# Kernel optimization log

Hardware: AMD Instinct MI355X
Metric: run time of the kernel (lower is better)

Reference implementation:

```python
import jax, jax.numpy as jnp
import numpy as np

B = 4; D = H = W = 28; C = 192; NH = 6; WS = 7; SS = 3
L = D * H * W; N = WS ** 3; HD = C // NH


def _rel_index():
    c = np.stack(np.meshgrid(np.arange(WS), np.arange(WS), np.arange(WS), indexing='ij')).reshape(3, -1)
    r = c[:, :, None] - c[:, None, :] + (WS - 1)
    return jnp.asarray(r[0] * (2 * WS - 1) ** 2 + r[1] * (2 * WS - 1) + r[2])  # (N,N)


def _attn_mask():
    img = np.zeros((D, H, W), np.float32)
    sl = (slice(0, -WS), slice(-WS, -SS), slice(-SS, None))
    cnt = 0
    for d in sl:
        for h in sl:
            for w in sl:
                img[d, h, w] = cnt; cnt += 1
    mw = img.reshape(D // WS, WS, H // WS, WS, W // WS, WS).transpose(0, 2, 4, 1, 3, 5).reshape(-1, N)
    am = mw[:, None, :] - mw[:, :, None]
    return jnp.asarray(np.where(am != 0, -100.0, 0.0).astype(np.float32))  # (nW,N,N)

REL_IDX = _rel_index()
ATTN_MASK = _attn_mask()


def _ln(x, g, b):
    m = x.mean(-1, keepdims=True)
    v = ((x - m) ** 2).mean(-1, keepdims=True)
    return (x - m) / jnp.sqrt(v + 1e-5) * g + b


def _window_partition(x):  # (B,D,H,W,C) -> (B*nW, N, C)
    x = x.reshape(B, D // WS, WS, H // WS, WS, W // WS, WS, C)
    return x.transpose(0, 1, 3, 5, 2, 4, 6, 7).reshape(-1, N, C)


def _window_reverse(w):  # (B*nW, N, C) -> (B,D,H,W,C)
    x = w.reshape(B, D // WS, H // WS, W // WS, WS, WS, WS, C)
    return x.transpose(0, 1, 4, 2, 5, 3, 6, 7).reshape(B, D, H, W, C)


def setup_inputs() -> dict:
    key = jax.random.key(0)
    ks = jax.random.split(key, 8)
    s = 0.02
    return {
        'x': jax.random.normal(ks[0], (B, L, C), jnp.float32),
        'norm1_g': jnp.ones((C,), jnp.float32), 'norm1_b': jnp.zeros((C,), jnp.float32),
        'qkv_w': jax.random.normal(ks[1], (3 * C, C), jnp.float32) * s,
        'qkv_b': jnp.zeros((3 * C,), jnp.float32),
        'proj_w': jax.random.normal(ks[2], (C, C), jnp.float32) * s,
        'proj_b': jnp.zeros((C,), jnp.float32),
        'rel_table': jax.random.normal(ks[3], ((2 * WS - 1) ** 3, NH), jnp.float32) * s,
        'norm2_g': jnp.ones((C,), jnp.float32), 'norm2_b': jnp.zeros((C,), jnp.float32),
        'fc1_w': jax.random.normal(ks[4], (4 * C, C), jnp.float32) * s,
        'fc1_b': jnp.zeros((4 * C,), jnp.float32),
        'fc2_w': jax.random.normal(ks[5], (C, 4 * C), jnp.float32) * s,
        'fc2_b': jnp.zeros((C,), jnp.float32),
    }


def reference(x, norm1_g, norm1_b, qkv_w, qkv_b, proj_w, proj_b, rel_table,
              norm2_g, norm2_b, fc1_w, fc1_b, fc2_w, fc2_b):
    shortcut = x
    h = _ln(x, norm1_g, norm1_b).reshape(B, D, H, W, C)
    h = jnp.roll(h, (-SS, -SS, -SS), axis=(1, 2, 3))
    xw = _window_partition(h)                                  # (B_, N, C)
    B_ = xw.shape[0]
    qkv = (xw @ qkv_w.T + qkv_b).reshape(B_, N, 3, NH, HD).transpose(2, 0, 3, 1, 4)
    q, k, v = qkv[0], qkv[1], qkv[2]                           # (B_, NH, N, HD)
    attn = jnp.einsum('bhnd,bhmd->bhnm', q * (HD ** -0.5), k)
    bias = rel_table[REL_IDX].transpose(2, 0, 1)               # (NH, N, N)
    attn = attn + bias[None]
    nW = ATTN_MASK.shape[0]
    attn = (attn.reshape(B, nW, NH, N, N) + ATTN_MASK[None, :, None]).reshape(B_, NH, N, N)
    attn = jax.nn.softmax(attn, axis=-1)
    out = jnp.einsum('bhnm,bhmd->bhnd', attn, v).transpose(0, 2, 1, 3).reshape(B_, N, C)
    out = out @ proj_w.T + proj_b
    h = _window_reverse(out)
    h = jnp.roll(h, (SS, SS, SS), axis=(1, 2, 3)).reshape(B, L, C)
    x = shortcut + h
    y = _ln(x, norm2_g, norm2_b)
    y = jax.nn.gelu(y @ fc1_w.T + fc1_b, approximate=False)
    return x + (y @ fc2_w.T + fc2_b)
```

## Files before the change

### kernel.cpp

```cpp
#include <hip/hip_runtime.h>

#define DEV __device__ __forceinline__

typedef __bf16 bf16x8 __attribute__((ext_vector_type(8)));
typedef float f32x4 __attribute__((ext_vector_type(4)));

DEV float bflo(unsigned int u) { union { unsigned int x; float f; } c; c.x = u << 16; return c.f; }
DEV unsigned short f2bf(float f) {
  union { float f; unsigned int u; } c; c.f = f;
  unsigned int u = c.u;
  return (unsigned short)((u + 0x7fffu + ((u >> 16) & 1u)) >> 16);
}
DEV unsigned int pkbf(float a, float b) {
  unsigned int r;
  asm("v_cvt_pk_bf16_f32 %0, %1, %2" : "=v"(r) : "v"(a), "v"(b));
  return r;
}
DEV float gelu_fast(float y) {
  float y2 = y * y;
  float z = y * fmaf(y2, 0.10294348f, 2.30220842f);
  float e = __builtin_amdgcn_exp2f(z);
  float r = __builtin_amdgcn_rcpf(e + 1.0f);
  return fmaf(-y, r, y);
}

DEV void gload16(const void* g, void* l) {
  __builtin_amdgcn_global_load_lds((const __attribute__((address_space(1))) void*)g,
                                   (__attribute__((address_space(3))) void*)l, 16, 0, 0);
}

__global__ __launch_bounds__(256) void wconv_all(const float* __restrict__ s0,
                                                 const float* __restrict__ s1,
                                                 const float* __restrict__ s2,
                                                 const float* __restrict__ s3,
                                                 unsigned short* __restrict__ dst) {
  int i = blockIdx.x * 256 + threadIdx.x;
  const float* src; int off, real;
  if (i < 122880)      { src = s0; off = i;          real = 110592; }
  else if (i < 172032) { src = s1; off = i - 122880; real = 36864; }
  else if (i < 319488) { src = s2; off = i - 172032; real = 147456; }
  else                 { src = s3; off = i - 319488; real = 147456; }
  dst[i] = (off < real) ? f2bf(src[off]) : (unsigned short)0;
}

__global__ __launch_bounds__(256) void bmt_kernel(const float* __restrict__ rel_table,
                                                  unsigned short* __restrict__ bmt4) {
  int wth = blockIdx.x;
  int wt = wth / 6, h = wth - wt * 6;
  int r = blockIdx.y;
  unsigned short* row = bmt4 + (((size_t)wth * 88 + r) * 352) * 4;
  for (int q = threadIdx.x; q < 352; q += 256) {
    int mb_q = 0, cls_q = 0;
    bool qv = q < 343;
    if (qv) {
      int ii_q = q / 49, rem_q = q - ii_q * 49;
      int jj_q = rem_q / 7, ww_q = rem_q - jj_q * 7;
      mb_q = ii_q * 169 + jj_q * 13 + ww_q;
      int cd_q = (wt & 4) ? (ii_q < 4 ? 1 : 2) : 0;
      int ch_q = (wt & 2) ? (jj_q < 4 ? 1 : 2) : 0;
      int cw_q = (wt & 1) ? (ww_q < 4 ? 1 : 2) : 0;
      cls_q = cd_q * 9 + ch_q * 3 + cw_q;
    }
    unsigned short ov[4];
#pragma unroll
    for (int i = 0; i < 4; i++) {
      int kk = 4 * r + i;
      float v;
      if (kk >= 343) v = -30000.f;
      else if (!qv) v = 0.f;
      else {
        int ii_k = kk / 49, rem_k = kk - ii_k * 49;
        int jj_k = rem_k / 7, ww_k = rem_k - jj_k * 7;
        int mb_k = ii_k * 169 + jj_k * 13 + ww_k;
        int cd_k = (wt & 4) ? (ii_k < 4 ? 1 : 2) : 0;
        int ch_k = (wt & 2) ? (jj_k < 4 ? 1 : 2) : 0;
        int cw_k = (wt & 1) ? (ww_k < 4 ? 1 : 2) : 0;
        int cls_k = cd_k * 9 + ch_k * 3 + cw_k;
        v = rel_table[(mb_q - mb_k + 1098) * 6 + h] * 1.4426950408889634f;
        if (cls_q != cls_k) v -= 144.26950408889634f;
      }
      ov[i] = f2bf(v);
    }
    unsigned int lo = (unsigned)ov[0] | ((unsigned)ov[1] << 16);
    unsigned int hi = (unsigned)ov[2] | ((unsigned)ov[3] << 16);
    *(uint2*)(row + q * 4) = make_uint2(lo, hi);
  }
}

__global__ __launch_bounds__(256) void ln_kernel(const float* __restrict__ x,
                                                 const float* __restrict__ g,
                                                 const float* __restrict__ b,
                                                 unsigned short* __restrict__ out) {
  int row = (blockIdx.x << 2) + (threadIdx.x >> 6);
  int lane = threadIdx.x & 63;
  int w_ = row / 343, n_ = row - w_ * 343;
  int bb = w_ >> 6, wrem = w_ & 63;
  int wd = wrem >> 4, wh = (wrem >> 2) & 3, ww = wrem & 3;
  int ii = n_ / 49, rem = n_ - ii * 49;
  int jj = rem / 7, kk = rem - jj * 7;
  int d = wd * 7 + ii + 3; if (d >= 28) d -= 28;
  int hh = wh * 7 + jj + 3; if (hh >= 28) hh -= 28;
  int wb = ww * 7 + kk + 3; if (wb >= 28) wb -= 28;
  const float* xr = x + ((size_t)bb * 21952 + (d * 28 + hh) * 28 + wb) * 192;
  float v0 = xr[lane], v1 = xr[lane + 64], v2 = xr[lane + 128];
  float s = v0 + v1 + v2;
  float sq = v0 * v0 + v1 * v1 + v2 * v2;
#pragma unroll
  for (int o = 32; o > 0; o >>= 1) {
    s += __shfl_xor(s, o, 64);
    sq += __shfl_xor(sq, o, 64);
  }
  float mean = s * (1.0f / 192.0f);
  float var = sq * (1.0f / 192.0f) - mean * mean;
  float rstd = rsqrtf(var + 1e-5f);
  unsigned short* orow = out + (size_t)row * 192;
  orow[lane]       = f2bf((v0 - mean) * rstd * g[lane] + b[lane]);
  orow[lane + 64]  = f2bf((v1 - mean) * rstd * g[lane + 64] + b[lane + 64]);
  orow[lane + 128] = f2bf((v2 - mean) * rstd * g[lane + 128] + b[lane + 128]);
}

__global__ __launch_bounds__(256) void gemm_qkv(
    const unsigned short* __restrict__ A, const unsigned short* __restrict__ W,
    const float* __restrict__ bias,
    unsigned short* __restrict__ oq, unsigned short* __restrict__ okk,
    unsigned short* __restrict__ ov) {
  __shared__ __align__(16) unsigned short As[2][128 * 64];
  __shared__ __align__(16) unsigned short Bs[2][128 * 64];
  const int K = 192;
  const int orig = blockIdx.x;
  const int xcd = orig & 7, off = orig >> 3;
  const int wgid = (xcd < 6 ? xcd * 429 : 2574 + (xcd - 6) * 428) + off;
  const int by = wgid / 5, bx = wgid - by * 5;
  const int bm = by << 7, bn = bx << 7;

  const int tid = threadIdx.x;
  const int lane = tid & 63;
  const int wv = tid >> 6;
  const int wr = wv >> 1, wc = wv & 1;
  const int l15 = lane & 15, l4 = lane >> 4;
  const int srow = lane >> 3;
  const int scole = ((lane & 7) ^ srow) << 3;

  f32x4 acc[4][4];
#pragma unroll
  for (int a = 0; a < 4; a++)
#pragma unroll
    for (int b2 = 0; b2 < 4; b2++) acc[a][b2] = (f32x4){0.f, 0.f, 0.f, 0.f};

  auto stage = [&](int kt, int buf) {
#pragma unroll
    for (int i = 0; i < 4; i++) {
      int c = (i << 2) + wv;
      int row = (c << 3) + srow;
      gload16(A + (size_t)(bm + row) * K + (kt << 6) + scole, &As[buf][c << 9]);
      gload16(W + (size_t)(bn + row) * K + (kt << 6) + scole, &Bs[buf][c << 9]);
    }
  };

  stage(0, 0);
  int cur = 0;
  for (int kt = 0; kt < 3; ++kt) {
    if (kt < 2) {
      stage(kt + 1, cur ^ 1);
      asm volatile("s_waitcnt vmcnt(8)" ::: "memory");
    } else {
      asm volatile("s_waitcnt vmcnt(0)" ::: "memory");
    }
    __builtin_amdgcn_s_barrier();
    __builtin_amdgcn_sched_barrier(0);
#pragma unroll
    for (int ks = 0; ks < 2; ks++) {
      bf16x8 af[4], bfr[4];
#pragma unroll
      for (int fm = 0; fm < 4; fm++) {
        int r = (wr << 6) + (fm << 4) + l15;
        int c = (ks << 2) + l4;
        af[fm] = *(const bf16x8*)(&As[cur][(r << 6) + ((c ^ (r & 7)) << 3)]);
      }
#pragma unroll
      for (int fn = 0; fn < 4; fn++) {
        int r = (wc << 6) + (fn << 4) + l15;
        int c = (ks << 2) + l4;
        bfr[fn] = *(const bf16x8*)(&Bs[cur][(r << 6) + ((c ^ (r & 7)) << 3)]);
      }
#pragma unroll
      for (int fm = 0; fm < 4; fm++)
#pragma unroll
        for (int fn = 0; fn < 4; fn++)
          acc[fm][fn] = __builtin_amdgcn_mfma_f32_16x16x32_bf16(bfr[fn], af[fm], acc[fm][fn], 0, 0, 0);
    }
    if (kt < 2) {
      __builtin_amdgcn_sched_barrier(0);
      __builtin_amdgcn_s_barrier();
      cur ^= 1;
    }
  }

#pragma unroll
  for (int fm = 0; fm < 4; fm++) {
    int gr = bm + (wr << 6) + (fm << 4) + l15;
    int w_ = gr / 343, n_ = gr - w_ * 343;
#pragma unroll
    for (int fn = 0; fn < 4; fn++) {
      int gc0 = bn + (wc << 6) + (fn << 4) + (l4 << 2);
      if (gc0 < 576) {
        float4 bv = *(const float4*)(bias + gc0);
        float v0 = acc[fm][fn][0] + bv.x, v1 = acc[fm][fn][1] + bv.y;
        float v2 = acc[fm][fn][2] + bv.z, v3 = acc[fm][fn][3] + bv.w;
        int which = gc0 / 192;
        int cc3 = gc0 - which * 192;
        int hh2 = cc3 >> 5, dd0 = cc3 & 31;
        size_t offo = ((size_t)(w_ * 6 + hh2) * 343 + n_) * 32 + dd0;
        if (which == 0) {
          const float sc = 0.17677669529663687f * 1.4426950408889634f;
          *(uint2*)(oq + offo) = make_uint2(pkbf(v0 * sc, v1 * sc), pkbf(v2 * sc, v3 * sc));
        } else if (which == 1) {
          *(uint2*)(okk + offo) = make_uint2(pkbf(v0, v1), pkbf(v2, v3));
        } else {
          *(uint2*)(ov + offo) = make_uint2(pkbf(v0, v1), pkbf(v2, v3));
        }
      }
    }
  }
}

__global__ __launch_bounds__(256) void proj_mlp(
    const unsigned short* __restrict__ A,
    const unsigned short* __restrict__ Wp, const float* __restrict__ bp,
    const float* __restrict__ x,
    const float* __restrict__ g2, const float* __restrict__ b2,
    const unsigned short* __restrict__ W1, const float* __restrict__ b1,
    const unsigned short* __restrict__ W2, const float* __restrict__ b2b,
    float* __restrict__ out) {
  __shared__ __align__(16) char smem[43008];
  unsigned short* pBs  = (unsigned short*)smem;
  unsigned short* pAs  = (unsigned short*)(smem + 24576);
  unsigned short* xw2s = (unsigned short*)smem;
  unsigned short* Hs   = (unsigned short*)(smem + 24576);
  float* red = (float*)(smem + 24576);

  const int tid = threadIdx.x, lane = tid & 63, wv = tid >> 6;
  const int l15 = lane & 15, l4 = lane >> 4;
  const int bm = blockIdx.x << 6;

  f32x4 acc[4][3];
#pragma unroll
  for (int a = 0; a < 4; a++)
#pragma unroll
    for (int b_ = 0; b_ < 3; b_++) acc[a][b_] = (f32x4){0.f, 0.f, 0.f, 0.f};

  for (int kt = 0; kt < 3; ++kt) {
    __syncthreads();
#pragma unroll
    for (int i = 0; i < 2; i++) {
      int u = (i << 8) + tid;
      int r = u >> 3, ch = u & 7;
      gload16(A + (size_t)(bm + r) * 192 + (kt << 6) + ((ch ^ (r & 7)) << 3), pAs + (u << 3));
    }
#pragma unroll
    for (int i = 0; i < 6; i++) {
      int u = (i << 8) + tid;
      int r = u >> 3, ch = u & 7;
      gload16(Wp + (size_t)r * 192 + (kt << 6) + ((ch ^ (r & 7)) << 3), pBs + (u << 3));
    }
    asm volatile("s_waitcnt vmcnt(0)" ::: "memory");
    __syncthreads();
#pragma unroll
    for (int ks = 0; ks < 2; ks++) {
      bf16x8 af[4], bfr[3];
#pragma unroll
      for (int fm = 0; fm < 4; fm++) {
        int r = (fm << 4) + l15;
        int c = (ks << 2) + l4;
        af[fm] = *(const bf16x8*)(pAs + (r << 6) + ((c ^ (r & 7)) << 3));
      }
#pragma unroll
      for (int fn = 0; fn < 3; fn++) {
        int rr = wv * 48 + (fn << 4) + l15;
        int c = (ks << 2) + l4;
        bfr[fn] = *(const bf16x8*)(pBs + (rr << 6) + ((c ^ (rr & 7)) << 3));
      }
#pragma unroll
      for (int fm = 0; fm < 4; fm++)
#pragma unroll
        for (int fn = 0; fn < 3; fn++)
          acc[fm][fn] = __builtin_amdgcn_mfma_f32_16x16x32_bf16(bfr[fn], af[fm], acc[fm][fn], 0, 0, 0);
    }
  }

  int orow[4];
#pragma unroll
  for (int fm = 0; fm < 4; fm++) {
    int gr = bm + (fm << 4) + l15;
    int w_ = gr / 343, n_ = gr - w_ * 343;
    int bb = w_ >> 6, wrem = w_ & 63;
    int wd = wrem >> 4, wh = (wrem >> 2) & 3, ww = wrem & 3;
    int ii = n_ / 49, rem = n_ - ii * 49;
    int jj = rem / 7, kk = rem - jj * 7;
    int d = wd * 7 + ii + 3; if (d >= 28) d -= 28;
    int hh = wh * 7 + jj + 3; if (hh >= 28) hh -= 28;
    int wb = ww * 7 + kk + 3; if (wb >= 28) wb -= 28;
    orow[fm] = ((bb * 21952 + (d * 28 + hh) * 28 + wb) * 192);
  }
  float ps[4], psq[4];
#pragma unroll
  for (int fm = 0; fm < 4; fm++) {
    float s = 0.f, sq = 0.f;
#pragma unroll
    for (int fn = 0; fn < 3; fn++) {
      int gc0 = wv * 48 + (fn << 4) + (l4 << 2);
      float4 bv = *(const float4*)(bp + gc0);
      float4 xv = *(const float4*)(x + (size_t)orow[fm] + gc0);
      acc[fm][fn][0] += bv.x + xv.x;
      acc[fm][fn][1] += bv.y + xv.y;
      acc[fm][fn][2] += bv.z + xv.z;
      acc[fm][fn][3] += bv.w + xv.w;
#pragma unroll
      for (int i = 0; i < 4; i++) {
        float v = acc[fm][fn][i];
        s += v; sq += v * v;
      }
    }
    ps[fm] = s; psq[fm] = sq;
  }
#pragma unroll
  for (int fm = 0; fm < 4; fm++) {
    ps[fm] += __shfl_xor(ps[fm], 16, 64);
    ps[fm] += __shfl_xor(ps[fm], 32, 64);
    psq[fm] += __shfl_xor(psq[fm], 16, 64);
    psq[fm] += __shfl_xor(psq[fm], 32, 64);
  }
  __syncthreads();
  if (l4 == 0) {
#pragma unroll
    for (int fm = 0; fm < 4; fm++) {
      int tr = (fm << 4) + l15;
      red[tr * 8 + wv] = ps[fm];
      red[tr * 8 + 4 + wv] = psq[fm];
    }
  }
  __syncthreads();
  if (tid < 64) {
    float s = red[tid * 8] + red[tid * 8 + 1] + red[tid * 8 + 2] + red[tid * 8 + 3];
    float sq = red[tid * 8 + 4] + red[tid * 8 + 5] + red[tid * 8 + 6] + red[tid * 8 + 7];
    float mean = s * (1.0f / 192.0f);
    float var = sq * (1.0f / 192.0f) - mean * mean;
    red[tid * 8] = mean;
    red[tid * 8 + 1] = rsqrtf(var + 1e-5f);
  }
  __syncthreads();
  unsigned int xnb[4][3][2];
#pragma unroll
  for (int fm = 0; fm < 4; fm++) {
    int tr = (fm << 4) + l15;
    float mean = red[tr * 8], rstd = red[tr * 8 + 1];
#pragma unroll
    for (int fn = 0; fn < 3; fn++) {
      int gc0 = wv * 48 + (fn << 4) + (l4 << 2);
      float4 gv = *(const float4*)(g2 + gc0);
      float4 b2v = *(const float4*)(b2 + gc0);
      float v0 = acc[fm][fn][0], v1 = acc[fm][fn][1];
      float v2 = acc[fm][fn][2], v3 = acc[fm][fn][3];
      xnb[fm][fn][0] = pkbf(v0, v1);
      xnb[fm][fn][1] = pkbf(v2, v3);
      float y0 = (v0 - mean) * rstd * gv.x + b2v.x;
      float y1 = (v1 - mean) * rstd * gv.y + b2v.y;
      float y2 = (v2 - mean) * rstd * gv.z + b2v.z;
      float y3 = (v3 - mean) * rstd * gv.w + b2v.w;
      int ch = gc0 >> 3;
      *(uint2*)(xw2s + tr * 192 + ((ch ^ (tr & 7)) << 3) + (gc0 & 7)) =
          make_uint2(pkbf(y0, y1), pkbf(y2, y3));
    }
  }
  __syncthreads();

  f32x4 acc2[4][3];
#pragma unroll
  for (int a = 0; a < 4; a++)
#pragma unroll
    for (int b_ = 0; b_ < 3; b_++) acc2[a][b_] = (f32x4){0.f, 0.f, 0.f, 0.f};

  for (int cc = 0; cc < 6; cc++) {
    f32x4 acc1[4][2];
#pragma unroll
    for (int a = 0; a < 4; a++) {
      acc1[a][0] = (f32x4){0.f, 0.f, 0.f, 0.f};
      acc1[a][1] = (f32x4){0.f, 0.f, 0.f, 0.f};
    }
#pragma unroll
    for (int ks = 0; ks < 6; ks++) {
      bf16x8 af[4], w1f[2];
#pragma unroll
      for (int fm = 0; fm < 4; fm++) {
        int r = (fm << 4) + l15;
        int ch = (ks << 2) + l4;
        af[fm] = *(const bf16x8*)(xw2s + r * 192 + ((ch ^ (r & 7)) << 3));
      }
#pragma unroll
      for (int fn = 0; fn < 2; fn++) {
        int hrow = (cc << 7) + (wv << 5) + (fn << 4) + l15;
        w1f[fn] = *(const bf16x8*)(W1 + (size_t)hrow * 192 + (ks << 5) + (l4 << 3));
      }
#pragma unroll
      for (int fm = 0; fm < 4; fm++)
#pragma unroll
        for (int fn = 0; fn < 2; fn++)
          acc1[fm][fn] = __builtin_amdgcn_mfma_f32_16x16x32_bf16(w1f[fn], af[fm], acc1[fm][fn], 0, 0, 0);
    }
    __syncthreads();
#pragma unroll
    for (int fm = 0; fm < 4; fm++) {
      int r = (fm << 4) + l15;
#pragma unroll
      for (int fn = 0; fn < 2; fn++) {
        int hc = (wv << 5) + (fn << 4) + (l4 << 2);
        float4 bv = *(const float4*)(b1 + (cc << 7) + hc);
        float g0 = gelu_fast(acc1[fm][fn][0] + bv.x);
        float g1 = gelu_fast(acc1[fm][fn][1] + bv.y);
        float g2_ = gelu_fast(acc1[fm][fn][2] + bv.z);
        float g3 = gelu_fast(acc1[fm][fn][3] + bv.w);
        *(uint2*)(Hs + r * 136 + hc) = make_uint2(pkbf(g0, g1), pkbf(g2_, g3));
      }
    }
    __syncthreads();
#pragma unroll
    for (int ks = 0; ks < 4; ks++) {
      bf16x8 hf[4], w2f[3];
#pragma unroll
      for (int fm = 0; fm < 4; fm++) {
        int r = (fm << 4) + l15;
        hf[fm] = *(const bf16x8*)(Hs + r * 136 + (ks << 5) + (l4 << 3));
      }
#pragma unroll
      for (int fn = 0; fn < 3; fn++) {
        int j = wv * 48 + (fn << 4) + l15;
        w2f[fn] = *(const bf16x8*)(W2 + (size_t)j * 768 + (cc << 7) + (ks << 5) + (l4 << 3));
      }
#pragma unroll
      for (int fm = 0; fm < 4; fm++)
#pragma unroll
        for (int fn = 0; fn < 3; fn++)
          acc2[fm][fn] = __builtin_amdgcn_mfma_f32_16x16x32_bf16(w2f[fn], hf[fm], acc2[fm][fn], 0, 0, 0);
    }
  }

#pragma unroll
  for (int fm = 0; fm < 4; fm++) {
#pragma unroll
    for (int fn = 0; fn < 3; fn++) {
      int gc0 = wv * 48 + (fn << 4) + (l4 << 2);
      float4 bv = *(const float4*)(b2b + gc0);
      float4 o;
      o.x = acc2[fm][fn][0] + bv.x + bflo(xnb[fm][fn][0] & 0xffffu);
      o.y = acc2[fm][fn][1] + bv.y + bflo(xnb[fm][fn][0] >> 16);
      o.z = acc2[fm][fn][2] + bv.z + bflo(xnb[fm][fn][1] & 0xffffu);
      o.w = acc2[fm][fn][3] + bv.w + bflo(xnb[fm][fn][1] >> 16);
      *(float4*)(out + (size_t)orow[fm] + gc0) = o;
    }
  }
}

__global__ __launch_bounds__(256) void attn_mfma(const unsigned short* __restrict__ q,
                                                 const unsigned short* __restrict__ k,
                                                 const unsigned short* __restrict__ v,
                                                 const unsigned short* __restrict__ bmt4,
                                                 unsigned short* __restrict__ out) {
  __shared__ __align__(16) unsigned short Ks[352 * 32];
  __shared__ __align__(16) unsigned short Vt[32 * 360];

  const int blk = blockIdx.x;
  const int h_ = blk >> 8;
  const int idx = blk & 255;
  const int cums[8] = {0, 108, 144, 180, 192, 228, 240, 252};
  int c = (idx >= 108) + (idx >= 144) + (idx >= 180) + (idx >= 192) +
          (idx >= 228) + (idx >= 240) + (idx >= 252);
  int r0 = idx - cums[c];
  int sh = (c & 2) ? 1 : 3, sw = (c & 1) ? 1 : 3;
  int p = ((c & 4) ? 1 : 3) * sh * sw;
  int b = r0 / p, q2 = r0 - b * p;
  int wd, wh, ww;
  if (c & 4) wd = 3; else { wd = q2 / (sh * sw); q2 -= wd * sh * sw; }
  if (c & 2) wh = 3; else { wh = q2 / sw; q2 -= wh * sw; }
  ww = (c & 1) ? 3 : q2;
  const int w_ = b * 64 + wd * 16 + wh * 4 + ww;
  const int wt = c;
  const int blkqkv = w_ * 6 + h_;

  const int t = threadIdx.x, lane = t & 63, wv = t >> 6;
  const int l15 = lane & 15, l4 = lane >> 4;
  const unsigned short* Qb = q + (size_t)blkqkv * (343 * 32);
  const unsigned short* Kb = k + (size_t)blkqkv * (343 * 32);
  const unsigned short* Vb = v + (size_t)blkqkv * (343 * 32);
  const unsigned short* bm4 = bmt4 + ((size_t)(wt * 6 + h_) * 88) * 352 * 4;

  for (int cc = t; cc < 1408; cc += 256) {
    int r = cc >> 2, ch = cc & 3;
    int swc = ch ^ ((r >> 1) & 3);
    uint4 val = make_uint4(0, 0, 0, 0);
    if (r < 343) val = *(const uint4*)(Kb + r * 32 + ch * 8);
    *(uint4*)(Ks + r * 32 + swc * 8) = val;
  }
#pragma unroll
  for (int ch = 0; ch < 4; ch++) {
    for (int n = t; n < 343; n += 256) {
      union { uint4 u4; unsigned short us[8]; } val;
      val.u4 = *(const uint4*)(Vb + n * 32 + ch * 8);
#pragma unroll
      for (int j = 0; j < 8; j++) Vt[(ch * 8 + j) * 360 + n] = val.us[j];
    }
  }
  for (int cc = t; cc < 288; cc += 256) {
    int d = cc / 9, n = 343 + (cc - d * 9);
    Vt[d * 360 + n] = 0;
  }
  __syncthreads();

  const int ksw = (l4 ^ ((l15 >> 1) & 3)) << 3;

  for (int tq = wv; tq < 22; tq += 4) {
    int qrow = tq * 16 + l15; if (qrow > 342) qrow = 342;
    bf16x8 qf = *(const bf16x8*)(Qb + qrow * 32 + l4 * 8);

    unsigned int u0[22], u1[22];
    float lsum = 0.f;
#pragma unroll
    for (int kt = 0; kt < 22; kt++) {
      bf16x8 kf = *(const bf16x8*)(Ks + (kt * 16 + l15) * 32 + ksw);
      f32x4 s = __builtin_amdgcn_mfma_f32_16x16x32_bf16(kf, qf, (f32x4){0.f, 0.f, 0.f, 0.f}, 0, 0, 0);
      const unsigned short* bp = bm4 + ((size_t)((kt << 2) + l4) * 352 + (tq << 4) + l15) * 4;
      uint2 bv = *(const uint2*)bp;
      float p0 = __builtin_amdgcn_exp2f(s[0] + bflo(bv.x & 0xffffu));
      float p1 = __builtin_amdgcn_exp2f(s[1] + bflo(bv.x >> 16));
      float p2 = __builtin_amdgcn_exp2f(s[2] + bflo(bv.y & 0xffffu));
      float p3 = __builtin_amdgcn_exp2f(s[3] + bflo(bv.y >> 16));
      lsum += (p0 + p1) + (p2 + p3);
      asm("v_cvt_pk_bf16_f32 %0, %1, %2" : "=v"(u0[kt]) : "v"(p0), "v"(p1));
      asm("v_cvt_pk_bf16_f32 %0, %1, %2" : "=v"(u1[kt]) : "v"(p2), "v"(p3));
    }
    lsum += __shfl_xor(lsum, 16, 64);
    lsum += __shfl_xor(lsum, 32, 64);
    float inv = 1.0f / lsum;

    f32x4 oacc0 = (f32x4){0.f, 0.f, 0.f, 0.f};
    f32x4 oacc1 = (f32x4){0.f, 0.f, 0.f, 0.f};
#pragma unroll
    for (int ck = 0; ck < 11; ck++) {
      unsigned int dw[4];
#pragma unroll
      for (int d = 0; d < 4; d++) {
        int src = l15 + 16 * ((d >> 1) + 2 * (l4 & 1));
        unsigned int x = __shfl((d & 1) ? u1[2 * ck] : u0[2 * ck], src, 64);
        unsigned int y = __shfl((d & 1) ? u1[2 * ck + 1] : u0[2 * ck + 1], src, 64);
        dw[d] = (l4 < 2) ? x : y;
      }
      union { unsigned int u[4]; bf16x8 v; } pc;
      pc.u[0] = dw[0]; pc.u[1] = dw[1]; pc.u[2] = dw[2]; pc.u[3] = dw[3];
      bf16x8 vf0 = *(const bf16x8*)(Vt + (size_t)l15 * 360 + ck * 32 + l4 * 8);
      bf16x8 vf1 = *(const bf16x8*)(Vt + (size_t)(16 + l15) * 360 + ck * 32 + l4 * 8);
      oacc0 = __builtin_amdgcn_mfma_f32_16x16x32_bf16(vf0, pc.v, oacc0, 0, 0, 0);
      oacc1 = __builtin_amdgcn_mfma_f32_16x16x32_bf16(vf1, pc.v, oacc1, 0, 0, 0);
    }

    int qg = tq * 16 + l15;
    if (qg < 343) {
      unsigned short* orow = out + ((size_t)w_ * 343 + qg) * 192 + h_ * 32;
      *(uint2*)(orow + (l4 << 2)) =
          make_uint2(pkbf(oacc0[0] * inv, oacc0[1] * inv), pkbf(oacc0[2] * inv, oacc0[3] * inv));
      *(uint2*)(orow + 16 + (l4 << 2)) =
          make_uint2(pkbf(oacc1[0] * inv, oacc1[1] * inv), pkbf(oacc1[2] * inv, oacc1[3] * inv));
    }
  }
}

extern "C" void kernel_launch(void* const* d_in, const int* in_sizes, int n_in,
                              void* d_out, int out_size, void* d_ws, size_t ws_size,
                              hipStream_t stream) {
  const float* x      = (const float*)d_in[0];
  const float* n1g    = (const float*)d_in[1];
  const float* n1b    = (const float*)d_in[2];
  const float* qkv_w  = (const float*)d_in[3];
  const float* qkv_b  = (const float*)d_in[4];
  const float* proj_w = (const float*)d_in[5];
  const float* proj_b = (const float*)d_in[6];
  const float* rel_t  = (const float*)d_in[7];
  const float* n2g    = (const float*)d_in[8];
  const float* n2b    = (const float*)d_in[9];
  const float* fc1_w  = (const float*)d_in[10];
  const float* fc1_b  = (const float*)d_in[11];
  const float* fc2_w  = (const float*)d_in[12];
  const float* fc2_b  = (const float*)d_in[13];

  char* ws = (char*)d_ws;
  if (ws_size < 147820032ull) return;
  unsigned short* WQKV  = (unsigned short*)(ws);
  unsigned short* WPROJ = (unsigned short*)(ws + 245760);
  unsigned short* WFC1  = (unsigned short*)(ws + 344064);
  unsigned short* WFC2  = (unsigned short*)(ws + 638976);
  unsigned short* XW    = (unsigned short*)(ws + 1032192);
  unsigned short* Q_    = (unsigned short*)(ws + 34750464);
  unsigned short* K_    = (unsigned short*)(ws + 68468736);
  unsigned short* V_    = (unsigned short*)(ws + 102187008);
  unsigned short* BMT4  = (unsigned short*)(ws + 135925248);
  float* OUT = (float*)d_out;

  wconv_all<<<2016, 256, 0, stream>>>(qkv_w, proj_w, fc1_w, fc2_w, WQKV);

  bmt_kernel<<<dim3(48, 88), 256, 0, stream>>>(rel_t, BMT4);

  ln_kernel<<<21952, 256, 0, stream>>>(x, n1g, n1b, XW);

  gemm_qkv<<<3430, 256, 0, stream>>>(XW, WQKV, qkv_b, Q_, K_, V_);

  attn_mfma<<<1536, 256, 0, stream>>>(Q_, K_, V_, BMT4, XW);

  proj_mlp<<<1372, 256, 0, stream>>>(XW, WPROJ, proj_b, x, n2g, n2b,
                                     WFC1, fc1_b, WFC2, fc2_b, OUT);
}
```

Before: 326.1 us.

## Double-buffer MLP hidden tile and prefetch W1/W2 fragments into registers

The MLP hidden-chunk buffer in shared memory is split into two alternating buffers, which removes one barrier per chunk. W1 and W2 fragments for each chunk are loaded into registers up front, so global loads can overlap the MFMA and GELU work. The chunk loop is fully unrolled and the kernel asks for two blocks per SIMD through launch bounds. In exchange it uses more LDS and many more VGPRs, which risks spills or lower occupancy.

```diff
diff --git a/kernel.cpp b/kernel.cpp
--- a/kernel.cpp
+++ b/kernel.cpp
@@ -224,7 +224,7 @@
   }
 }
 
-__global__ __launch_bounds__(256) void proj_mlp(
+__global__ __launch_bounds__(256, 2) void proj_mlp(
     const unsigned short* __restrict__ A,
     const unsigned short* __restrict__ Wp, const float* __restrict__ bp,
     const float* __restrict__ x,
@@ -232,11 +232,12 @@
     const unsigned short* __restrict__ W1, const float* __restrict__ b1,
     const unsigned short* __restrict__ W2, const float* __restrict__ b2b,
     float* __restrict__ out) {
-  __shared__ __align__(16) char smem[43008];
+  __shared__ __align__(16) char smem[59392];
   unsigned short* pBs  = (unsigned short*)smem;
   unsigned short* pAs  = (unsigned short*)(smem + 24576);
   unsigned short* xw2s = (unsigned short*)smem;
-  unsigned short* Hs   = (unsigned short*)(smem + 24576);
+  unsigned short* Hs0  = (unsigned short*)(smem + 24576);
+  unsigned short* Hs1  = (unsigned short*)(smem + 41984);
   float* red = (float*)(smem + 24576);
 
   const int tid = threadIdx.x, lane = tid & 63, wv = tid >> 6;
@@ -380,7 +381,17 @@
 #pragma unroll
     for (int b_ = 0; b_ < 3; b_++) acc2[a][b_] = (f32x4){0.f, 0.f, 0.f, 0.f};
 
+#pragma unroll
   for (int cc = 0; cc < 6; cc++) {
+    unsigned short* Hc = (cc & 1) ? Hs1 : Hs0;
+    bf16x8 w1r[2][6];
+#pragma unroll
+    for (int fn = 0; fn < 2; fn++)
+#pragma unroll
+      for (int ks = 0; ks < 6; ks++) {
+        int hrow = (cc << 7) + (wv << 5) + (fn << 4) + l15;
+        w1r[fn][ks] = *(const bf16x8*)(W1 + (size_t)hrow * 192 + (ks << 5) + (l4 << 3));
+      }
     f32x4 acc1[4][2];
 #pragma unroll
     for (int a = 0; a < 4; a++) {
@@ -389,7 +400,7 @@
     }
 #pragma unroll
     for (int ks = 0; ks < 6; ks++) {
-      bf16x8 af[4], w1f[2];
+      bf16x8 af[4];
 #pragma unroll
       for (int fm = 0; fm < 4; fm++) {
         int r = (fm << 4) + l15;
@@ -397,17 +408,19 @@
         af[fm] = *(const bf16x8*)(xw2s + r * 192 + ((ch ^ (r & 7)) << 3));
       }
 #pragma unroll
-      for (int fn = 0; fn < 2; fn++) {
-        int hrow = (cc << 7) + (wv << 5) + (fn << 4) + l15;
-        w1f[fn] = *(const bf16x8*)(W1 + (size_t)hrow * 192 + (ks << 5) + (l4 << 3));
-      }
-#pragma unroll
       for (int fm = 0; fm < 4; fm++)
 #pragma unroll
         for (int fn = 0; fn < 2; fn++)
-          acc1[fm][fn] = __builtin_amdgcn_mfma_f32_16x16x32_bf16(w1f[fn], af[fm], acc1[fm][fn], 0, 0, 0);
-    }
-    __syncthreads();
+          acc1[fm][fn] = __builtin_amdgcn_mfma_f32_16x16x32_bf16(w1r[fn][ks], af[fm], acc1[fm][fn], 0, 0, 0);
+    }
+    bf16x8 w2r[3][4];
+#pragma unroll
+    for (int fn = 0; fn < 3; fn++)
+#pragma unroll
+      for (int ks = 0; ks < 4; ks++) {
+        int j = wv * 48 + (fn << 4) + l15;
+        w2r[fn][ks] = *(const bf16x8*)(W2 + (size_t)j * 768 + (cc << 7) + (ks << 5) + (l4 << 3));
+      }
 #pragma unroll
     for (int fm = 0; fm < 4; fm++) {
       int r = (fm << 4) + l15;
@@ -419,28 +432,23 @@
         float g1 = gelu_fast(acc1[fm][fn][1] + bv.y);
         float g2_ = gelu_fast(acc1[fm][fn][2] + bv.z);
         float g3 = gelu_fast(acc1[fm][fn][3] + bv.w);
-        *(uint2*)(Hs + r * 136 + hc) = make_uint2(pkbf(g0, g1), pkbf(g2_, g3));
+        *(uint2*)(Hc + r * 136 + hc) = make_uint2(pkbf(g0, g1), pkbf(g2_, g3));
       }
     }
     __syncthreads();
 #pragma unroll
     for (int ks = 0; ks < 4; ks++) {
-      bf16x8 hf[4], w2f[3];
+      bf16x8 hf[4];
 #pragma unroll
       for (int fm = 0; fm < 4; fm++) {
         int r = (fm << 4) + l15;
-        hf[fm] = *(const bf16x8*)(Hs + r * 136 + (ks << 5) + (l4 << 3));
-      }
-#pragma unroll
-      for (int fn = 0; fn < 3; fn++) {
-        int j = wv * 48 + (fn << 4) + l15;
-        w2f[fn] = *(const bf16x8*)(W2 + (size_t)j * 768 + (cc << 7) + (ks << 5) + (l4 << 3));
+        hf[fm] = *(const bf16x8*)(Hc + r * 136 + (ks << 5) + (l4 << 3));
       }
 #pragma unroll
       for (int fm = 0; fm < 4; fm++)
 #pragma unroll
         for (int fn = 0; fn < 3; fn++)
-          acc2[fm][fn] = __builtin_amdgcn_mfma_f32_16x16x32_bf16(w2f[fn], hf[fm], acc2[fm][fn], 0, 0, 0);
+          acc2[fm][fn] = __builtin_amdgcn_mfma_f32_16x16x32_bf16(w2r[fn][ks], hf[fm], acc2[fm][fn], 0, 0, 0);
     }
   }
 
```

Measured after the change: 314.5 us. -3.6%, faster.

## Stage full proj A tile in LDS once and read proj weights from global

Applied to the files above, without the earlier changes.

The projection GEMM in proj_mlp no longer loops over three K-tiles that each stage A and Wp slices in shared memory. It now loads the whole 64x192 A tile into LDS once, swizzled to match the later xw2 layout, and reads Wp fragments straight from global/L2. The residual x loads are issued early so they overlap the MFMA loop. Shared memory shrinks slightly and launch bounds request 3 blocks per CU, which can push more registers into spills given the prefetched xv registers.

```diff
diff --git a/kernel.cpp b/kernel.cpp
--- a/kernel.cpp
+++ b/kernel.cpp
@@ -224,7 +224,7 @@
   }
 }
 
-__global__ __launch_bounds__(256) void proj_mlp(
+__global__ __launch_bounds__(256, 3) void proj_mlp(
     const unsigned short* __restrict__ A,
     const unsigned short* __restrict__ Wp, const float* __restrict__ bp,
     const float* __restrict__ x,
@@ -232,61 +232,14 @@
     const unsigned short* __restrict__ W1, const float* __restrict__ b1,
     const unsigned short* __restrict__ W2, const float* __restrict__ b2b,
     float* __restrict__ out) {
-  __shared__ __align__(16) char smem[43008];
-  unsigned short* pBs  = (unsigned short*)smem;
-  unsigned short* pAs  = (unsigned short*)(smem + 24576);
-  unsigned short* xw2s = (unsigned short*)smem;
-  unsigned short* Hs   = (unsigned short*)(smem + 24576);
+  __shared__ __align__(16) char smem[41984];
+  unsigned short* As = (unsigned short*)smem;
+  unsigned short* Hs = (unsigned short*)(smem + 24576);
   float* red = (float*)(smem + 24576);
 
   const int tid = threadIdx.x, lane = tid & 63, wv = tid >> 6;
   const int l15 = lane & 15, l4 = lane >> 4;
   const int bm = blockIdx.x << 6;
-
-  f32x4 acc[4][3];
-#pragma unroll
-  for (int a = 0; a < 4; a++)
-#pragma unroll
-    for (int b_ = 0; b_ < 3; b_++) acc[a][b_] = (f32x4){0.f, 0.f, 0.f, 0.f};
-
-  for (int kt = 0; kt < 3; ++kt) {
-    __syncthreads();
-#pragma unroll
-    for (int i = 0; i < 2; i++) {
-      int u = (i << 8) + tid;
-      int r = u >> 3, ch = u & 7;
-      gload16(A + (size_t)(bm + r) * 192 + (kt << 6) + ((ch ^ (r & 7)) << 3), pAs + (u << 3));
-    }
-#pragma unroll
-    for (int i = 0; i < 6; i++) {
-      int u = (i << 8) + tid;
-      int r = u >> 3, ch = u & 7;
-      gload16(Wp + (size_t)r * 192 + (kt << 6) + ((ch ^ (r & 7)) << 3), pBs + (u << 3));
-    }
-    asm volatile("s_waitcnt vmcnt(0)" ::: "memory");
-    __syncthreads();
-#pragma unroll
-    for (int ks = 0; ks < 2; ks++) {
-      bf16x8 af[4], bfr[3];
-#pragma unroll
-      for (int fm = 0; fm < 4; fm++) {
-        int r = (fm << 4) + l15;
-        int c = (ks << 2) + l4;
-        af[fm] = *(const bf16x8*)(pAs + (r << 6) + ((c ^ (r & 7)) << 3));
-      }
-#pragma unroll
-      for (int fn = 0; fn < 3; fn++) {
-        int rr = wv * 48 + (fn << 4) + l15;
-        int c = (ks << 2) + l4;
-        bfr[fn] = *(const bf16x8*)(pBs + (rr << 6) + ((c ^ (rr & 7)) << 3));
-      }
-#pragma unroll
-      for (int fm = 0; fm < 4; fm++)
-#pragma unroll
-        for (int fn = 0; fn < 3; fn++)
-          acc[fm][fn] = __builtin_amdgcn_mfma_f32_16x16x32_bf16(bfr[fn], af[fm], acc[fm][fn], 0, 0, 0);
-    }
-  }
 
   int orow[4];
 #pragma unroll
@@ -302,6 +255,51 @@
     int wb = ww * 7 + kk + 3; if (wb >= 28) wb -= 28;
     orow[fm] = ((bb * 21952 + (d * 28 + hh) * 28 + wb) * 192);
   }
+
+#pragma unroll
+  for (int i = 0; i < 6; i++) {
+    int idx = (i << 8) + tid;
+    int r = idx / 24, c = idx - r * 24;
+    gload16(A + (size_t)(bm + r) * 192 + ((c ^ (r & 7)) << 3), As + r * 192 + (c << 3));
+  }
+  asm volatile("s_waitcnt vmcnt(0)" ::: "memory");
+  __builtin_amdgcn_s_barrier();
+
+  float4 xv[4][3];
+#pragma unroll
+  for (int fm = 0; fm < 4; fm++)
+#pragma unroll
+    for (int fn = 0; fn < 3; fn++) {
+      int gc0 = wv * 48 + (fn << 4) + (l4 << 2);
+      xv[fm][fn] = *(const float4*)(x + (size_t)orow[fm] + gc0);
+    }
+
+  f32x4 acc[4][3];
+#pragma unroll
+  for (int a = 0; a < 4; a++)
+#pragma unroll
+    for (int b_ = 0; b_ < 3; b_++) acc[a][b_] = (f32x4){0.f, 0.f, 0.f, 0.f};
+#pragma unroll
+  for (int ks = 0; ks < 6; ks++) {
+    bf16x8 af[4], wpf[3];
+#pragma unroll
+    for (int fm = 0; fm < 4; fm++) {
+      int r = (fm << 4) + l15;
+      int ch = (ks << 2) + l4;
+      af[fm] = *(const bf16x8*)(As + r * 192 + ((ch ^ (r & 7)) << 3));
+    }
+#pragma unroll
+    for (int fn = 0; fn < 3; fn++) {
+      int rr = wv * 48 + (fn << 4) + l15;
+      wpf[fn] = *(const bf16x8*)(Wp + (size_t)rr * 192 + (ks << 5) + (l4 << 3));
+    }
+#pragma unroll
+    for (int fm = 0; fm < 4; fm++)
+#pragma unroll
+      for (int fn = 0; fn < 3; fn++)
+        acc[fm][fn] = __builtin_amdgcn_mfma_f32_16x16x32_bf16(wpf[fn], af[fm], acc[fm][fn], 0, 0, 0);
+  }
+
   float ps[4], psq[4];
 #pragma unroll
   for (int fm = 0; fm < 4; fm++) {
@@ -310,11 +308,10 @@
     for (int fn = 0; fn < 3; fn++) {
       int gc0 = wv * 48 + (fn << 4) + (l4 << 2);
       float4 bv = *(const float4*)(bp + gc0);
-      float4 xv = *(const float4*)(x + (size_t)orow[fm] + gc0);
-      acc[fm][fn][0] += bv.x + xv.x;
-      acc[fm][fn][1] += bv.y + xv.y;
-      acc[fm][fn][2] += bv.z + xv.z;
-      acc[fm][fn][3] += bv.w + xv.w;
+      acc[fm][fn][0] += bv.x + xv[fm][fn].x;
+      acc[fm][fn][1] += bv.y + xv[fm][fn].y;
+      acc[fm][fn][2] += bv.z + xv[fm][fn].z;
+      acc[fm][fn][3] += bv.w + xv[fm][fn].w;
 #pragma unroll
       for (int i = 0; i < 4; i++) {
         float v = acc[fm][fn][i];
@@ -368,7 +365,7 @@
       float y2 = (v2 - mean) * rstd * gv.z + b2v.z;
       float y3 = (v3 - mean) * rstd * gv.w + b2v.w;
       int ch = gc0 >> 3;
-      *(uint2*)(xw2s + tr * 192 + ((ch ^ (tr & 7)) << 3) + (gc0 & 7)) =
+      *(uint2*)(As + tr * 192 + ((ch ^ (tr & 7)) << 3) + (gc0 & 7)) =
           make_uint2(pkbf(y0, y1), pkbf(y2, y3));
     }
   }
@@ -394,7 +391,7 @@
       for (int fm = 0; fm < 4; fm++) {
         int r = (fm << 4) + l15;
         int ch = (ks << 2) + l4;
-        af[fm] = *(const bf16x8*)(xw2s + r * 192 + ((ch ^ (r & 7)) << 3));
+        af[fm] = *(const bf16x8*)(As + r * 192 + ((ch ^ (r & 7)) << 3));
       }
 #pragma unroll
       for (int fn = 0; fn < 2; fn++) {
```

After: 318.6 us. 1.02x faster.
